# Kernel optimization log

Hardware: AMD Instinct MI355X
Metric: run time of the kernel (lower is better)

## Reference

```python
import jax, jax.numpy as jnp
import numpy as np
from jax import lax

BETA = 0.9
THRESHOLD = 1.0
SLOPE = 25.0
TIME_STEPS = 50


@jax.custom_vjp
def spike(u):
    # Heaviside forward; fast_sigmoid surrogate backward
    return (u > 0).astype(u.dtype)

def _spike_fwd(u):
    return spike(u), u

def _spike_bwd(u, g):
    return (g / (SLOPE * jnp.abs(u) + 1.0) ** 2,)

spike.defvjp(_spike_fwd, _spike_bwd)


def setup_inputs() -> dict:
    key = jax.random.key(0)
    k = jax.random.split(key, 5)
    B, D_IN, D_H, D_OUT = 1024, 1024, 2048, 256
    return {
        "x": jax.random.normal(k[0], (B, D_IN), jnp.float32),
        "W1": jax.random.normal(k[1], (D_H, D_IN), jnp.float32) / np.sqrt(D_IN),
        "b1": jax.random.normal(k[2], (D_H,), jnp.float32) * 0.01,
        "W2": jax.random.normal(k[3], (D_OUT, D_H), jnp.float32) / np.sqrt(D_H),
        "b2": jax.random.normal(k[4], (D_OUT,), jnp.float32) * 0.01,
    }


def reference(x, W1, b1, W2, b2):
    # fc1(x) is constant across time steps (static input) -> hoist out of scan
    cur1 = x @ W1.T + b1  # [B, H]
    B = x.shape[0]
    H, O = W1.shape[0], W2.shape[0]
    dt = x.dtype

    def step(carry, _):
        mem1, mem2, h_sum, out_sum = carry
        # snntorch Leaky, subtract reset: reset based on PREVIOUS mem, detached
        reset1 = lax.stop_gradient((mem1 > THRESHOLD).astype(dt))
        mem1 = BETA * mem1 + cur1 - reset1 * THRESHOLD
        spk1 = spike(mem1 - THRESHOLD)
        cur2 = spk1 @ W2.T + b2  # [B, O]
        reset2 = lax.stop_gradient((mem2 > THRESHOLD).astype(dt))
        mem2 = BETA * mem2 + cur2 - reset2 * THRESHOLD
        spk2 = spike(mem2 - THRESHOLD)
        return (mem1, mem2, h_sum + spk1, out_sum + spk2), None

    init = (jnp.zeros((B, H), dt), jnp.zeros((B, O), dt),
            jnp.zeros((B, H), dt), jnp.zeros((B, O), dt))
    (mem1, mem2, h_sum, out_sum), _ = lax.scan(step, init, None, length=TIME_STEPS)
    return (h_sum, out_sum)
```

## Files before the change

### kernel.cpp

```cpp
#include <hip/hip_runtime.h>
#include <stdint.h>


#define BATCH 1024
#define DIN   1024
#define DH    2048
#define DOUT  256
#define TSTEPS 50
#define QS    131072.0f
#define QINVS 7.62939453125e-6f

typedef __bf16 bf16x8 __attribute__((ext_vector_type(8)));
typedef float  f32x4  __attribute__((ext_vector_type(4)));
typedef int    i32x4  __attribute__((ext_vector_type(4)));
typedef int    i32x16 __attribute__((ext_vector_type(16)));

__device__ __forceinline__ uint16_t f32_bf16_rne(float f) {
  uint32_t u = __float_as_uint(f);
  uint32_t r = u + 0x7FFFu + ((u >> 16) & 1u);
  return (uint16_t)(r >> 16);
}

__device__ __forceinline__ i32x4 expand16(uint32_t s) {
  i32x4 r;
  r[0] = (int)((( s        & 0xFu) * 0x00204081u) & 0x01010101u);
  r[1] = (int)((((s >>  4) & 0xFu) * 0x00204081u) & 0x01010101u);
  r[2] = (int)((((s >>  8) & 0xFu) * 0x00204081u) & 0x01010101u);
  r[3] = (int)((((s >> 12) & 0xFu) * 0x00204081u) & 0x01010101u);
  return r;
}

__global__ void prep_kernel(const float* __restrict__ x, const float* __restrict__ W1,
                            const float* __restrict__ W2,
                            uint16_t* __restrict__ PXh, uint16_t* __restrict__ PXl,
                            uint16_t* __restrict__ PWh, uint16_t* __restrict__ PWl,
                            int8_t* __restrict__ PB) {
  int bid = blockIdx.x;
  if (bid < 1536) {
    const float* src;
    uint16_t *dh, *dl;
    int m, ko; size_t M;
    if (bid < 512) {
      int t = bid * 256 + threadIdx.x;
      m = t >> 7; ko = t & 127; M = 1024;
      src = x + (size_t)m * DIN + ko * 8;
      dh = PXh; dl = PXl;
    } else {
      int t = (bid - 512) * 256 + threadIdx.x;
      m = t >> 7; ko = t & 127; M = 2048;
      src = W1 + (size_t)m * DIN + ko * 8;
      dh = PWh; dl = PWl;
    }
    float4 a = *(const float4*)(src);
    float4 b = *(const float4*)(src + 4);
    float v[8] = {a.x, a.y, a.z, a.w, b.x, b.y, b.z, b.w};
    uint16_t h[8], l[8];
#pragma unroll
    for (int j = 0; j < 8; ++j) {
      h[j] = f32_bf16_rne(v[j]);
      l[j] = f32_bf16_rne(v[j] - __uint_as_float((uint32_t)h[j] << 16));
    }
    size_t o = ((size_t)ko * M + m) * 8;
    *(uint4*)(dh + o) = make_uint4(h[0] | (h[1] << 16), h[2] | (h[3] << 16),
                                   h[4] | (h[5] << 16), h[6] | (h[7] << 16));
    *(uint4*)(dl + o) = make_uint4(l[0] | (l[1] << 16), l[2] | (l[3] << 16),
                                   l[4] | (l[5] << 16), l[6] | (l[7] << 16));
  } else {
    int t = (bid - 1536) * 256 + threadIdx.x;
    int k0 = (t & 127) * 16;
    int n = t >> 7;
    uint32_t hw[4], lw[4];
#pragma unroll
    for (int g = 0; g < 4; ++g) {
      float4 v = *(const float4*)(W2 + (size_t)n * DH + k0 + g * 4);
      float vv[4] = {v.x, v.y, v.z, v.w};
      uint32_t hb = 0, lb = 0;
#pragma unroll
      for (int j = 0; j < 4; ++j) {
        int q = (int)rintf(vv[j] * QS);
        int h = (q + 128) >> 8;
        int l = q - (h << 8);
        hb |= ((uint32_t)(uint8_t)(int8_t)h) << (8 * j);
        lb |= ((uint32_t)(uint8_t)(int8_t)l) << (8 * j);
      }
      hw[g] = hb; lw[g] = lb;
    }
    int kc = k0 >> 5, kh = (k0 >> 4) & 1, nb = n >> 5;
    int lane = (n & 31) + 32 * kh;
    size_t off = (((size_t)(kc * 8 + nb) * 2 + 0) * 64 + lane) * 16;
    *(uint4*)(PB + off)        = make_uint4(hw[0], hw[1], hw[2], hw[3]);
    *(uint4*)(PB + off + 1024) = make_uint4(lw[0], lw[1], lw[2], lw[3]);
  }
}

__global__ __launch_bounds__(256, 2) void gemm1_kernel(
    const uint16_t* __restrict__ PXh, const uint16_t* __restrict__ PXl,
    const uint16_t* __restrict__ PWh, const uint16_t* __restrict__ PWl,
    const float* __restrict__ bias, float* __restrict__ C) {
  const int N = DH;
  int tid = threadIdx.x;
  int lane = tid & 63, wave = tid >> 6;
  int wm = (wave >> 1) * 32, wn = (wave & 1) * 32;
  int m0 = blockIdx.x * 64 + wm;
  int n0 = blockIdx.y * 64 + wn;
  int rf = lane & 15;
  int ko = lane >> 4;
  const int AK = 4 * 1024 * 8;
  const int BK = 4 * 2048 * 8;

  const uint16_t* axh = PXh + ((size_t)ko * 1024 + m0 + rf) * 8;
  const uint16_t* axl = PXl + ((size_t)ko * 1024 + m0 + rf) * 8;
  const uint16_t* bwh = PWh + ((size_t)ko * 2048 + n0 + rf) * 8;
  const uint16_t* bwl = PWl + ((size_t)ko * 2048 + n0 + rf) * 8;

  f32x4 acc[2][2] = {};
  bf16x8 ah[2][2], al[2][2], bh[2][2], bl[2][2];
#pragma unroll
  for (int s = 0; s < 2; ++s) {
#pragma unroll
    for (int i = 0; i < 2; ++i) {
      ah[s][i] = *(const bf16x8*)(axh + i * 128);
      al[s][i] = *(const bf16x8*)(axl + i * 128);
      bh[s][i] = *(const bf16x8*)(bwh + i * 128);
      bl[s][i] = *(const bf16x8*)(bwl + i * 128);
    }
    axh += AK; axl += AK; bwh += BK; bwl += BK;
  }
  __builtin_amdgcn_sched_barrier(0);

  for (int kc0 = 0; kc0 < 32; kc0 += 2) {
#pragma unroll
    for (int u = 0; u < 2; ++u) {
#pragma unroll
      for (int i = 0; i < 2; ++i)
#pragma unroll
        for (int j = 0; j < 2; ++j) {
          acc[i][j] = __builtin_amdgcn_mfma_f32_16x16x32_bf16(ah[u][i], bh[u][j], acc[i][j], 0, 0, 0);
          acc[i][j] = __builtin_amdgcn_mfma_f32_16x16x32_bf16(ah[u][i], bl[u][j], acc[i][j], 0, 0, 0);
          acc[i][j] = __builtin_amdgcn_mfma_f32_16x16x32_bf16(al[u][i], bh[u][j], acc[i][j], 0, 0, 0);
        }
      __builtin_amdgcn_sched_barrier(0);
#pragma unroll
      for (int i = 0; i < 2; ++i) {
        ah[u][i] = *(const bf16x8*)(axh + i * 128);
        al[u][i] = *(const bf16x8*)(axl + i * 128);
        bh[u][i] = *(const bf16x8*)(bwh + i * 128);
        bl[u][i] = *(const bf16x8*)(bwl + i * 128);
      }
      axh += AK; axl += AK; bwh += BK; bwl += BK;
      __builtin_amdgcn_sched_barrier(0);
    }
  }

  int cq = (lane >> 4) * 4;
#pragma unroll
  for (int j = 0; j < 2; ++j) {
    int col = n0 + j * 16 + rf;
    float bv = bias[col];
#pragma unroll
    for (int i = 0; i < 2; ++i) {
      size_t row = m0 + i * 16 + cq;
      float* cp = C + row * N + col;
#pragma unroll
      for (int r = 0; r < 4; ++r) cp[(size_t)r * N] = acc[i][j][r] + bv;
    }
  }
}

__global__ __launch_bounds__(512, 2) void gemm2_kernel(
    const uint16_t* __restrict__ PAb, const int8_t* __restrict__ PB,
    const float* __restrict__ bias, float* __restrict__ C, int RB) {
  int tid = threadIdx.x;
  int lane = tid & 63, wave = tid >> 6;
  int wmh = wave >> 2;
  int wnq = wave & 3;
  int bx = blockIdx.x;
  int mb0 = bx * 4 + wmh * 2;

  const uint16_t* pa = PAb + (size_t)mb0 * 64 + lane;
  const int8_t*   pb = PB + ((size_t)wnq * 4 * 64 + lane) * 16;
  size_t strideA = (size_t)RB * 64;

  i32x16 acch[2][2] = {};
  i32x16 accl[2][2] = {};

  uint32_t abit[4][2];
  i32x4 bb[4][4];
#pragma unroll
  for (int u = 0; u < 4; ++u) {
    abit[u][0] = pa[0];
    abit[u][1] = pa[64];
    bb[u][0] = *(const i32x4*)(pb);
    bb[u][1] = *(const i32x4*)(pb + 1024);
    bb[u][2] = *(const i32x4*)(pb + 2048);
    bb[u][3] = *(const i32x4*)(pb + 3072);
    pa += strideA; pb += 16384;
  }
  __builtin_amdgcn_sched_barrier(0);

  for (int kc0 = 0; kc0 < 64; kc0 += 4) {
#pragma unroll
    for (int u = 0; u < 4; ++u) {
      i32x4 a0 = expand16(abit[u][0]);
      i32x4 a1 = expand16(abit[u][1]);
      acch[0][0] = __builtin_amdgcn_mfma_i32_32x32x32_i8(a0, bb[u][0], acch[0][0], 0, 0, 0);
      accl[0][0] = __builtin_amdgcn_mfma_i32_32x32x32_i8(a0, bb[u][1], accl[0][0], 0, 0, 0);
      acch[0][1] = __builtin_amdgcn_mfma_i32_32x32x32_i8(a0, bb[u][2], acch[0][1], 0, 0, 0);
      accl[0][1] = __builtin_amdgcn_mfma_i32_32x32x32_i8(a0, bb[u][3], accl[0][1], 0, 0, 0);
      acch[1][0] = __builtin_amdgcn_mfma_i32_32x32x32_i8(a1, bb[u][0], acch[1][0], 0, 0, 0);
      accl[1][0] = __builtin_amdgcn_mfma_i32_32x32x32_i8(a1, bb[u][1], accl[1][0], 0, 0, 0);
      acch[1][1] = __builtin_amdgcn_mfma_i32_32x32x32_i8(a1, bb[u][2], acch[1][1], 0, 0, 0);
      accl[1][1] = __builtin_amdgcn_mfma_i32_32x32x32_i8(a1, bb[u][3], accl[1][1], 0, 0, 0);
      __builtin_amdgcn_sched_barrier(0);
      abit[u][0] = pa[0];
      abit[u][1] = pa[64];
      bb[u][0] = *(const i32x4*)(pb);
      bb[u][1] = *(const i32x4*)(pb + 1024);
      bb[u][2] = *(const i32x4*)(pb + 2048);
      bb[u][3] = *(const i32x4*)(pb + 3072);
      pa += strideA; pb += 16384;
      __builtin_amdgcn_sched_barrier(0);
    }
  }

  int rm = lane & 31, half = lane >> 5;
#pragma unroll
  for (int mi = 0; mi < 2; ++mi)
#pragma unroll
    for (int ni = 0; ni < 2; ++ni) {
      int col = wnq * 64 + ni * 32 + rm;
      float bv = bias[col];
#pragma unroll
      for (int r = 0; r < 16; ++r) {
        int row = bx * 128 + wmh * 64 + mi * 32 + (r & 3) + 8 * (r >> 2) + 4 * half;
        int q = acch[mi][ni][r] * 256 + accl[mi][ni][r];
        C[(size_t)row * DOUT + col] = (float)q * QINVS + bv;
      }
    }
}

__global__ void lif1_kernel(const float* __restrict__ cur1, float* __restrict__ mem1,
                            uint16_t* __restrict__ PAb, float* __restrict__ hsum,
                            int tc, int init, int save_mem, int RB) {
#pragma clang fp contract(off)
  int idx = blockIdx.x * 256 + threadIdx.x;
  int b = idx & 1023;
  int h0 = (idx >> 10) * 16;
  size_t e0 = (size_t)b * DH + h0;

  float m[16], c[16], hs[16];
#pragma unroll
  for (int g = 0; g < 4; ++g) {
    float4 v = *(const float4*)(cur1 + e0 + g * 4);
    c[g * 4] = v.x; c[g * 4 + 1] = v.y; c[g * 4 + 2] = v.z; c[g * 4 + 3] = v.w;
  }
#pragma unroll
  for (int v = 0; v < 16; ++v) { m[v] = 0.0f; hs[v] = 0.0f; }
  if (!init) {
#pragma unroll
    for (int g = 0; g < 4; ++g) {
      float4 v = *(const float4*)(mem1 + e0 + g * 4);
      m[g * 4] = v.x; m[g * 4 + 1] = v.y; m[g * 4 + 2] = v.z; m[g * 4 + 3] = v.w;
    }
  }

  int kc = h0 >> 5, kh = (h0 >> 4) & 1;
  int lane = (b & 31) + 32 * kh;
  uint16_t* pab = PAb + ((size_t)kc * RB + (b >> 5)) * 64 + lane;

  for (int t = 0; t < tc; ++t) {
    uint32_t w = 0;
#pragma unroll
    for (int v = 0; v < 16; ++v) {
      float r = (m[v] > 1.0f) ? 1.0f : 0.0f;
      m[v] = 0.9f * m[v] + c[v] - r;
      bool s = (m[v] - 1.0f) > 0.0f;
      hs[v] += s ? 1.0f : 0.0f;
      w |= (s ? 1u : 0u) << v;
    }
    *pab = (uint16_t)w;
    pab += 32 * 64;
  }

  if (save_mem) {
#pragma unroll
    for (int g = 0; g < 4; ++g)
      *(float4*)(mem1 + e0 + g * 4) = make_float4(m[g * 4], m[g * 4 + 1], m[g * 4 + 2], m[g * 4 + 3]);
  }
  if (init) {
#pragma unroll
    for (int g = 0; g < 4; ++g)
      *(float4*)(hsum + e0 + g * 4) = make_float4(hs[g * 4], hs[g * 4 + 1], hs[g * 4 + 2], hs[g * 4 + 3]);
  } else {
#pragma unroll
    for (int g = 0; g < 4; ++g) {
      float4 v = *(float4*)(hsum + e0 + g * 4);
      v.x += hs[g * 4]; v.y += hs[g * 4 + 1]; v.z += hs[g * 4 + 2]; v.w += hs[g * 4 + 3];
      *(float4*)(hsum + e0 + g * 4) = v;
    }
  }
}

__global__ void lif2_kernel(const float* __restrict__ cur2, float* __restrict__ mem2,
                            float* __restrict__ osum, int tc, int init, int save_mem) {
#pragma clang fp contract(off)
  int idx = blockIdx.x * 256 + threadIdx.x;
  int e = idx * 4;
  float m[4], os[4];
  if (init) { m[0] = m[1] = m[2] = m[3] = 0.0f; }
  else { float4 v = *(const float4*)(mem2 + e); m[0] = v.x; m[1] = v.y; m[2] = v.z; m[3] = v.w; }
  os[0] = os[1] = os[2] = os[3] = 0.0f;
  for (int t = 0; t < tc; ++t) {
    float4 cv = *(const float4*)(cur2 + (size_t)t * (BATCH * DOUT) + e);
    float c[4] = {cv.x, cv.y, cv.z, cv.w};
#pragma unroll
    for (int v = 0; v < 4; ++v) {
      float r = (m[v] > 1.0f) ? 1.0f : 0.0f;
      m[v] = 0.9f * m[v] + c[v] - r;
      os[v] += ((m[v] - 1.0f) > 0.0f) ? 1.0f : 0.0f;
    }
  }
  if (save_mem) *(float4*)(mem2 + e) = make_float4(m[0], m[1], m[2], m[3]);
  if (init) {
    *(float4*)(osum + e) = make_float4(os[0], os[1], os[2], os[3]);
  } else {
    float4 v = *(float4*)(osum + e);
    v.x += os[0]; v.y += os[1]; v.z += os[2]; v.w += os[3];
    *(float4*)(osum + e) = v;
  }
}

extern "C" void kernel_launch(void* const* d_in, const int* in_sizes, int n_in,
                              void* d_out, int out_size, void* d_ws, size_t ws_size,
                              hipStream_t stream) {
  const float* x  = (const float*)d_in[0];
  const float* W1 = (const float*)d_in[1];
  const float* b1 = (const float*)d_in[2];
  const float* W2 = (const float*)d_in[3];
  const float* b2 = (const float*)d_in[4];
  float* out = (float*)d_out;
  char* ws = (char*)d_ws;

  const size_t fixed = 36 * 1024 * 1024;
  const size_t perT  = 262144 + 1048576;
  int tc = 10;
  if (ws_size >= fixed + 50ull * perT) tc = 50;
  else if (ws_size >= fixed + 25ull * perT) tc = 25;
  int nchunk = TSTEPS / tc;
  int RB = tc * 32;

  size_t off = 0;
  auto alloc = [&](size_t b) { size_t p = off; off = (off + b + 255) & ~(size_t)255; return p; };
  uint16_t* PXh  = (uint16_t*)(ws + alloc(2097152));
  uint16_t* PXl  = (uint16_t*)(ws + alloc(2097152));
  uint16_t* PWh  = (uint16_t*)(ws + alloc(4194304));
  uint16_t* PWl  = (uint16_t*)(ws + alloc(4194304));
  int8_t*   PB   = (int8_t*)(ws + alloc(1048576 + 262144));
  float*    cur1 = (float*)(ws + alloc(8388608));
  float*    mem1 = (float*)(ws + alloc(8388608));
  float*    mem2 = (float*)(ws + alloc(1048576));
  uint16_t* PAb  = (uint16_t*)(ws + alloc((size_t)tc * 262144 + 4ull * RB * 128));
  float*    cur2c = (float*)(ws + alloc((size_t)tc * BATCH * DOUT * 4));

  if (nchunk > 1) {
    hipMemsetAsync(mem1, 0, 8388608, stream);
    hipMemsetAsync(mem2, 0, 1048576, stream);
  }

  prep_kernel<<<1664, 256, 0, stream>>>(x, W1, W2, PXh, PXl, PWh, PWl, PB);

  gemm1_kernel<<<dim3(16, 32), 256, 0, stream>>>(PXh, PXl, PWh, PWl, b1, cur1);

  int save = (nchunk > 1) ? 1 : 0;
  for (int c = 0; c < nchunk; ++c) {
    int init = (c == 0) ? 1 : 0;
    lif1_kernel<<<(BATCH * DH) / (256 * 16), 256, 0, stream>>>(
        cur1, mem1, PAb, out, tc, init, save, RB);
    gemm2_kernel<<<(tc * BATCH) / 128, 512, 0, stream>>>(
        PAb, PB, b2, cur2c, RB);
    lif2_kernel<<<(BATCH * DOUT) / (256 * 4), 256, 0, stream>>>(
        cur2c, mem2, out + BATCH * DH, tc, init, save);
  }
}
```

Baseline: 206.2 us.

## Retile gemm2 into 256-thread blocks with 4x1 wave tiles and pipelined A expansion

Splits the gemm2 grid across two N blocks with 256 threads each. Each wave now computes four M subtiles against one 32-wide N column pair (high and low int8 halves) instead of a 2x2 tile. The A spike-bit expansion is double-buffered so the next step's expansion overlaps the current MFMAs. Each wave loads less B and more A bits; A loads are duplicated across the two N blocks, while per-wave register pressure changes.

```diff
diff --git a/kernel.cpp b/kernel.cpp
--- a/kernel.cpp
+++ b/kernel.cpp
@@ -167,76 +167,70 @@
   }
 }
 
-__global__ __launch_bounds__(512, 2) void gemm2_kernel(
+__global__ __launch_bounds__(256, 2) void gemm2_kernel(
     const uint16_t* __restrict__ PAb, const int8_t* __restrict__ PB,
     const float* __restrict__ bias, float* __restrict__ C, int RB) {
   int tid = threadIdx.x;
   int lane = tid & 63, wave = tid >> 6;
-  int wmh = wave >> 2;
-  int wnq = wave & 3;
-  int bx = blockIdx.x;
-  int mb0 = bx * 4 + wmh * 2;
-
-  const uint16_t* pa = PAb + (size_t)mb0 * 64 + lane;
-  const int8_t*   pb = PB + ((size_t)wnq * 4 * 64 + lane) * 16;
+  int bxn = blockIdx.x;
+  int bym = blockIdx.y;
+
+  const uint16_t* pa = PAb + (size_t)(bym * 4) * 64 + lane;
+  const int8_t*   pb = PB + ((size_t)(bxn * 4 + wave) * 2 * 64 + lane) * 16;
   size_t strideA = (size_t)RB * 64;
 
-  i32x16 acch[2][2] = {};
-  i32x16 accl[2][2] = {};
-
-  uint32_t abit[4][2];
-  i32x4 bb[4][4];
+  i32x16 acch[4] = {};
+  i32x16 accl[4] = {};
+
+  uint16_t abit[4][4];
+  i32x4 bbh[4], bbl[4];
+  i32x4 aexp[2][4];
+
 #pragma unroll
   for (int u = 0; u < 4; ++u) {
-    abit[u][0] = pa[0];
-    abit[u][1] = pa[64];
-    bb[u][0] = *(const i32x4*)(pb);
-    bb[u][1] = *(const i32x4*)(pb + 1024);
-    bb[u][2] = *(const i32x4*)(pb + 2048);
-    bb[u][3] = *(const i32x4*)(pb + 3072);
+#pragma unroll
+    for (int mi = 0; mi < 4; ++mi) abit[u][mi] = pa[mi * 64];
+    bbh[u] = *(const i32x4*)(pb);
+    bbl[u] = *(const i32x4*)(pb + 1024);
     pa += strideA; pb += 16384;
   }
+#pragma unroll
+  for (int mi = 0; mi < 4; ++mi) aexp[0][mi] = expand16(abit[0][mi]);
   __builtin_amdgcn_sched_barrier(0);
 
   for (int kc0 = 0; kc0 < 64; kc0 += 4) {
 #pragma unroll
     for (int u = 0; u < 4; ++u) {
-      i32x4 a0 = expand16(abit[u][0]);
-      i32x4 a1 = expand16(abit[u][1]);
-      acch[0][0] = __builtin_amdgcn_mfma_i32_32x32x32_i8(a0, bb[u][0], acch[0][0], 0, 0, 0);
-      accl[0][0] = __builtin_amdgcn_mfma_i32_32x32x32_i8(a0, bb[u][1], accl[0][0], 0, 0, 0);
-      acch[0][1] = __builtin_amdgcn_mfma_i32_32x32x32_i8(a0, bb[u][2], acch[0][1], 0, 0, 0);
-      accl[0][1] = __builtin_amdgcn_mfma_i32_32x32x32_i8(a0, bb[u][3], accl[0][1], 0, 0, 0);
-      acch[1][0] = __builtin_amdgcn_mfma_i32_32x32x32_i8(a1, bb[u][0], acch[1][0], 0, 0, 0);
-      accl[1][0] = __builtin_amdgcn_mfma_i32_32x32x32_i8(a1, bb[u][1], accl[1][0], 0, 0, 0);
-      acch[1][1] = __builtin_amdgcn_mfma_i32_32x32x32_i8(a1, bb[u][2], acch[1][1], 0, 0, 0);
-      accl[1][1] = __builtin_amdgcn_mfma_i32_32x32x32_i8(a1, bb[u][3], accl[1][1], 0, 0, 0);
+      const int p = u & 1;
+#pragma unroll
+      for (int mi = 0; mi < 4; ++mi) aexp[p ^ 1][mi] = expand16(abit[(u + 1) & 3][mi]);
+#pragma unroll
+      for (int mi = 0; mi < 4; ++mi) {
+        acch[mi] = __builtin_amdgcn_mfma_i32_32x32x32_i8(aexp[p][mi], bbh[u], acch[mi], 0, 0, 0);
+        accl[mi] = __builtin_amdgcn_mfma_i32_32x32x32_i8(aexp[p][mi], bbl[u], accl[mi], 0, 0, 0);
+      }
       __builtin_amdgcn_sched_barrier(0);
-      abit[u][0] = pa[0];
-      abit[u][1] = pa[64];
-      bb[u][0] = *(const i32x4*)(pb);
-      bb[u][1] = *(const i32x4*)(pb + 1024);
-      bb[u][2] = *(const i32x4*)(pb + 2048);
-      bb[u][3] = *(const i32x4*)(pb + 3072);
+#pragma unroll
+      for (int mi = 0; mi < 4; ++mi) abit[u][mi] = pa[mi * 64];
+      bbh[u] = *(const i32x4*)(pb);
+      bbl[u] = *(const i32x4*)(pb + 1024);
       pa += strideA; pb += 16384;
       __builtin_amdgcn_sched_barrier(0);
     }
   }
 
   int rm = lane & 31, half = lane >> 5;
-#pragma unroll
-  for (int mi = 0; mi < 2; ++mi)
-#pragma unroll
-    for (int ni = 0; ni < 2; ++ni) {
-      int col = wnq * 64 + ni * 32 + rm;
-      float bv = bias[col];
-#pragma unroll
-      for (int r = 0; r < 16; ++r) {
-        int row = bx * 128 + wmh * 64 + mi * 32 + (r & 3) + 8 * (r >> 2) + 4 * half;
-        int q = acch[mi][ni][r] * 256 + accl[mi][ni][r];
-        C[(size_t)row * DOUT + col] = (float)q * QINVS + bv;
-      }
-    }
+  int col = bxn * 128 + wave * 32 + rm;
+  float bv = bias[col];
+#pragma unroll
+  for (int mi = 0; mi < 4; ++mi) {
+#pragma unroll
+    for (int r = 0; r < 16; ++r) {
+      int row = bym * 128 + mi * 32 + (r & 3) + 8 * (r >> 2) + 4 * half;
+      int q = acch[mi][r] * 256 + accl[mi][r];
+      C[(size_t)row * DOUT + col] = (float)q * QINVS + bv;
+    }
+  }
 }
 
 __global__ void lif1_kernel(const float* __restrict__ cur1, float* __restrict__ mem1,
@@ -376,7 +370,7 @@
     int init = (c == 0) ? 1 : 0;
     lif1_kernel<<<(BATCH * DH) / (256 * 16), 256, 0, stream>>>(
         cur1, mem1, PAb, out, tc, init, save, RB);
-    gemm2_kernel<<<(tc * BATCH) / 128, 512, 0, stream>>>(
+    gemm2_kernel<<<dim3(2, (tc * BATCH) / 128), 256, 0, stream>>>(
         PAb, PB, b2, cur2c, RB);
     lif2_kernel<<<(BATCH * DOUT) / (256 * 4), 256, 0, stream>>>(
         cur2c, mem2, out + BATCH * DH, tc, init, save);
```

Result: faster. 196.8 us (-4.6%).

## Shrink gemm2 per-wave tile and split output columns across grid y

Applied to the files above, without the earlier changes.

Restructures gemm2 so each wave computes a 32-row by 64-column tile instead of 64x64. Output columns are spread over a second grid dimension, giving 256-thread blocks with launch bounds raised to three blocks per CU. The A bit expansion is now software-pipelined one step ahead, so the expand overlaps the MFMAs. This lowers register pressure and raises parallelism. The cost is less A and B reuse per wave, so the same spike bits are reloaded by four column blocks.

```diff
diff --git a/kernel.cpp b/kernel.cpp
--- a/kernel.cpp
+++ b/kernel.cpp
@@ -167,53 +167,48 @@
   }
 }
 
-__global__ __launch_bounds__(512, 2) void gemm2_kernel(
+__global__ __launch_bounds__(256, 3) void gemm2_kernel(
     const uint16_t* __restrict__ PAb, const int8_t* __restrict__ PB,
     const float* __restrict__ bias, float* __restrict__ C, int RB) {
   int tid = threadIdx.x;
   int lane = tid & 63, wave = tid >> 6;
-  int wmh = wave >> 2;
-  int wnq = wave & 3;
-  int bx = blockIdx.x;
-  int mb0 = bx * 4 + wmh * 2;
-
-  const uint16_t* pa = PAb + (size_t)mb0 * 64 + lane;
-  const int8_t*   pb = PB + ((size_t)wnq * 4 * 64 + lane) * 16;
+  int bxm = blockIdx.x;
+  int by  = blockIdx.y;
+
+  const uint16_t* pa = PAb + (size_t)(bxm * 4 + wave) * 64 + lane;
+  const int8_t*   pb = PB + ((size_t)by * 4 * 64 + lane) * 16;
   size_t strideA = (size_t)RB * 64;
 
-  i32x16 acch[2][2] = {};
-  i32x16 accl[2][2] = {};
-
-  uint32_t abit[4][2];
+  i32x16 acch[2] = {};
+  i32x16 accl[2] = {};
+
+  uint16_t abit[4];
   i32x4 bb[4][4];
+  i32x4 aexp[2];
+
 #pragma unroll
   for (int u = 0; u < 4; ++u) {
-    abit[u][0] = pa[0];
-    abit[u][1] = pa[64];
+    abit[u] = pa[0];
     bb[u][0] = *(const i32x4*)(pb);
     bb[u][1] = *(const i32x4*)(pb + 1024);
     bb[u][2] = *(const i32x4*)(pb + 2048);
     bb[u][3] = *(const i32x4*)(pb + 3072);
     pa += strideA; pb += 16384;
   }
+  aexp[0] = expand16(abit[0]);
   __builtin_amdgcn_sched_barrier(0);
 
   for (int kc0 = 0; kc0 < 64; kc0 += 4) {
 #pragma unroll
     for (int u = 0; u < 4; ++u) {
-      i32x4 a0 = expand16(abit[u][0]);
-      i32x4 a1 = expand16(abit[u][1]);
-      acch[0][0] = __builtin_amdgcn_mfma_i32_32x32x32_i8(a0, bb[u][0], acch[0][0], 0, 0, 0);
-      accl[0][0] = __builtin_amdgcn_mfma_i32_32x32x32_i8(a0, bb[u][1], accl[0][0], 0, 0, 0);
-      acch[0][1] = __builtin_amdgcn_mfma_i32_32x32x32_i8(a0, bb[u][2], acch[0][1], 0, 0, 0);
-      accl[0][1] = __builtin_amdgcn_mfma_i32_32x32x32_i8(a0, bb[u][3], accl[0][1], 0, 0, 0);
-      acch[1][0] = __builtin_amdgcn_mfma_i32_32x32x32_i8(a1, bb[u][0], acch[1][0], 0, 0, 0);
-      accl[1][0] = __builtin_amdgcn_mfma_i32_32x32x32_i8(a1, bb[u][1], accl[1][0], 0, 0, 0);
-      acch[1][1] = __builtin_amdgcn_mfma_i32_32x32x32_i8(a1, bb[u][2], acch[1][1], 0, 0, 0);
-      accl[1][1] = __builtin_amdgcn_mfma_i32_32x32x32_i8(a1, bb[u][3], accl[1][1], 0, 0, 0);
+      const int p = u & 1;
+      aexp[p ^ 1] = expand16(abit[(u + 1) & 3]);
+      acch[0] = __builtin_amdgcn_mfma_i32_32x32x32_i8(aexp[p], bb[u][0], acch[0], 0, 0, 0);
+      accl[0] = __builtin_amdgcn_mfma_i32_32x32x32_i8(aexp[p], bb[u][1], accl[0], 0, 0, 0);
+      acch[1] = __builtin_amdgcn_mfma_i32_32x32x32_i8(aexp[p], bb[u][2], acch[1], 0, 0, 0);
+      accl[1] = __builtin_amdgcn_mfma_i32_32x32x32_i8(aexp[p], bb[u][3], accl[1], 0, 0, 0);
       __builtin_amdgcn_sched_barrier(0);
-      abit[u][0] = pa[0];
-      abit[u][1] = pa[64];
+      abit[u] = pa[0];
       bb[u][0] = *(const i32x4*)(pb);
       bb[u][1] = *(const i32x4*)(pb + 1024);
       bb[u][2] = *(const i32x4*)(pb + 2048);
@@ -225,18 +220,16 @@
 
   int rm = lane & 31, half = lane >> 5;
 #pragma unroll
-  for (int mi = 0; mi < 2; ++mi)
-#pragma unroll
-    for (int ni = 0; ni < 2; ++ni) {
-      int col = wnq * 64 + ni * 32 + rm;
-      float bv = bias[col];
-#pragma unroll
-      for (int r = 0; r < 16; ++r) {
-        int row = bx * 128 + wmh * 64 + mi * 32 + (r & 3) + 8 * (r >> 2) + 4 * half;
-        int q = acch[mi][ni][r] * 256 + accl[mi][ni][r];
-        C[(size_t)row * DOUT + col] = (float)q * QINVS + bv;
-      }
-    }
+  for (int ni = 0; ni < 2; ++ni) {
+    int col = by * 64 + ni * 32 + rm;
+    float bv = bias[col];
+#pragma unroll
+    for (int r = 0; r < 16; ++r) {
+      int row = bxm * 128 + wave * 32 + (r & 3) + 8 * (r >> 2) + 4 * half;
+      int q = acch[ni][r] * 256 + accl[ni][r];
+      C[(size_t)row * DOUT + col] = (float)q * QINVS + bv;
+    }
+  }
 }
 
 __global__ void lif1_kernel(const float* __restrict__ cur1, float* __restrict__ mem1,
@@ -376,7 +369,7 @@
     int init = (c == 0) ? 1 : 0;
     lif1_kernel<<<(BATCH * DH) / (256 * 16), 256, 0, stream>>>(
         cur1, mem1, PAb, out, tc, init, save, RB);
-    gemm2_kernel<<<(tc * BATCH) / 128, 512, 0, stream>>>(
+    gemm2_kernel<<<dim3((tc * BATCH) / 128, 4), 256, 0, stream>>>(
         PAb, PB, b2, cur2c, RB);
     lif2_kernel<<<(BATCH * DOUT) / (256 * 4), 256, 0, stream>>>(
         cur2c, mem2, out + BATCH * DH, tc, init, save);
```

Result: no change. 209.3 us (+1.5%).
